# Performance work log

Measured on AMD Instinct MI355X. Metric: run time of the kernel, lower is better.

## Reference

```python
import jax, jax.numpy as jnp
import numpy as np

B, T, I, H, O = 1024, 512, 4, 128, 4


def setup_inputs() -> dict:
    key = jax.random.key(0)
    ks = jax.random.split(key, 7)
    s_ih = 1.0 / np.sqrt(H)
    return {
        "x": jax.random.normal(ks[0], (B, T, I), dtype=jnp.float32),
        "W_ih": jax.random.uniform(ks[1], (4 * H, I), jnp.float32, -s_ih, s_ih),
        "W_hh": jax.random.uniform(ks[2], (4 * H, H), jnp.float32, -s_ih, s_ih),
        "b_ih": jax.random.uniform(ks[3], (4 * H,), jnp.float32, -s_ih, s_ih),
        "b_hh": jax.random.uniform(ks[4], (4 * H,), jnp.float32, -s_ih, s_ih),
        "W_fc": jax.random.uniform(ks[5], (O, H), jnp.float32, -s_ih, s_ih),
        "b_fc": jax.random.uniform(ks[6], (O,), jnp.float32, -s_ih, s_ih),
    }


def _lstm_last_hidden(x, W_ih, W_hh, b_ih, b_hh):
    """Single-layer LSTM (PyTorch gate order i,f,g,o); returns h_T of shape (B,H)."""
    Bn = x.shape[0]
    Hn = W_hh.shape[1]
    # Precompute input contributions for all timesteps: (T, B, 4H)
    x_proj = jnp.einsum('bti,gi->tbg', x, W_ih) + (b_ih + b_hh)

    def step(carry, xp_t):
        h, c = carry
        gates = xp_t + h @ W_hh.T  # (B, 4H)
        i_g, f_g, g_g, o_g = jnp.split(gates, 4, axis=-1)
        i_g = jax.nn.sigmoid(i_g)
        f_g = jax.nn.sigmoid(f_g)
        g_g = jnp.tanh(g_g)
        o_g = jax.nn.sigmoid(o_g)
        c = f_g * c + i_g * g_g
        h = o_g * jnp.tanh(c)
        return (h, c), None

    h0 = jnp.zeros((Bn, Hn), x.dtype)
    c0 = jnp.zeros((Bn, Hn), x.dtype)
    (h_T, _), _ = jax.lax.scan(step, (h0, c0), x_proj)
    return h_T


def reference(x, W_ih, W_hh, b_ih, b_hh, W_fc, b_fc):
    # out, _ = lstm(x); last = out[:, -1]; dropout (eval/identity); fc(last)
    last = _lstm_last_hidden(x, W_ih, W_hh, b_ih, b_hh)
    return last @ W_fc.T + b_fc
```

## Files before the change

kernel.cpp:

```cpp
#include <hip/hip_runtime.h>
#include <hip/hip_bf16.h>


#define Tlen 512
#define Iin  4
#define Hdim 128
#define Odim 4

#define SB0() __builtin_amdgcn_sched_barrier(0)

typedef __attribute__((ext_vector_type(8))) short bf16x8;
typedef __attribute__((ext_vector_type(4))) float f32x4;
typedef __attribute__((ext_vector_type(2))) unsigned uint2v;
typedef __attribute__((ext_vector_type(4))) unsigned uint4v;

static __device__ __forceinline__ short f2bf(float f) {
  union { float f; unsigned u; } v; v.f = f;
  unsigned u = v.u;
  return (short)((u + 0x7FFFu + ((u >> 16) & 1u)) >> 16);
}
static __device__ __forceinline__ unsigned cvt_pk_bf16(float lo, float hi) {
  unsigned r;
  asm("v_cvt_pk_bf16_f32 %0, %1, %2" : "=v"(r) : "v"(lo), "v"(hi));
  return r;
}
static __device__ __forceinline__ float ex2(float x) { return __builtin_amdgcn_exp2f(x); }
static __device__ __forceinline__ float rcp_(float x) { return __builtin_amdgcn_rcpf(x); }

#define MFMA __builtin_amdgcn_mfma_f32_16x16x32_bf16

__global__ __launch_bounds__(512) void lstm_kernel(
    const float* __restrict__ x, const float* __restrict__ W_ih,
    const float* __restrict__ W_hh, const float* __restrict__ b_ih,
    const float* __restrict__ b_hh, const float* __restrict__ W_fc,
    const float* __restrict__ b_fc, float* __restrict__ out) {
  __shared__ alignas(16) short Albuf[2][16][168];
  __shared__ float hfin[16][Hdim];

  const int tid  = threadIdx.x;
  const int wid  = tid >> 6;
  const int lane = tid & 63;
  const int m16  = lane & 15;
  const int grp  = lane >> 4;
  const int bbase = blockIdx.x * 16;
  const float L2E = 1.4426950408889634f;

  bf16x8 Wf[4][4];
  bf16x8 Wx[4];
  f32x4  c0v[4];
#pragma unroll
  for (int q = 0; q < 4; ++q) {
    const float sc = (q == 2) ? 2.0f * L2E : L2E;
    const int gm = q * 128 + wid * 16 + m16;
#pragma unroll
    for (int kc = 0; kc < 4; ++kc) {
      const float* src = W_hh + (size_t)gm * Hdim + kc * 32 + grp * 8;
      bf16x8 w;
#pragma unroll
      for (int e = 0; e < 8; ++e) w[e] = f2bf(src[e] * sc);
      Wf[q][kc] = w;
    }
    bf16x8 w4 = {0, 0, 0, 0, 0, 0, 0, 0};
    if (grp == 0) {
#pragma unroll
      for (int e = 0; e < 4; ++e) w4[e] = f2bf(W_ih[gm * Iin + e] * sc);
    }
    Wx[q] = w4;
#pragma unroll
    for (int r = 0; r < 4; ++r) {
      const int gr = q * 128 + wid * 16 + grp * 4 + r;
      c0v[q][r] = (b_ih[gr] + b_hh[gr]) * sc;
    }
  }

  for (int i = tid; i < 2 * 16 * 168; i += 512) ((short*)Albuf)[i] = 0;

  const float* xrow = x + (size_t)(bbase + m16) * (Tlen * Iin);

  f32x4 acc0, acc1, acc2, acc3;
  {
    f32x4 xv = *(const f32x4*)xrow;
    uint4v u;
    u[0] = cvt_pk_bf16(xv[0], xv[1]);
    u[1] = cvt_pk_bf16(xv[2], xv[3]);
    u[2] = 0; u[3] = 0;
    union { uint4v uu; bf16x8 v; } cst; cst.uu = u;
    acc0 = MFMA(Wx[0], cst.v, c0v[0], 0, 0, 0);
    acc1 = MFMA(Wx[1], cst.v, c0v[1], 0, 0, 0);
    acc2 = MFMA(Wx[2], cst.v, c0v[2], 0, 0, 0);
    acc3 = MFMA(Wx[3], cst.v, c0v[3], 0, 0, 0);
  }

  float c4[4] = {0.f, 0.f, 0.f, 0.f};
  float hl[4] = {0.f, 0.f, 0.f, 0.f};
  __syncthreads();

  for (int t = 0; t < Tlen; ++t) {
    const int cur = t & 1, nxt = cur ^ 1;

    bf16x8 b0 = *(const bf16x8*)&Albuf[cur][m16][ 0 + grp * 8];
    bf16x8 b1 = *(const bf16x8*)&Albuf[cur][m16][32 + grp * 8];
    bf16x8 b2 = *(const bf16x8*)&Albuf[cur][m16][64 + grp * 8];
    bf16x8 b3 = *(const bf16x8*)&Albuf[cur][m16][96 + grp * 8];
    const int tn = (t + 1 < Tlen) ? (t + 1) : (Tlen - 1);
    f32x4 xv = *(const f32x4*)(xrow + (size_t)tn * Iin);

    acc0 = MFMA(Wf[0][0], b0, acc0, 0, 0, 0);
    acc0 = MFMA(Wf[0][1], b1, acc0, 0, 0, 0);
    acc0 = MFMA(Wf[0][2], b2, acc0, 0, 0, 0);
    acc0 = MFMA(Wf[0][3], b3, acc0, 0, 0, 0);
    acc1 = MFMA(Wf[1][0], b0, acc1, 0, 0, 0);
    acc1 = MFMA(Wf[1][1], b1, acc1, 0, 0, 0);
    acc1 = MFMA(Wf[1][2], b2, acc1, 0, 0, 0);
    acc1 = MFMA(Wf[1][3], b3, acc1, 0, 0, 0);
    SB0();
    f32x4 si;
    {
      float p0 = 1.0f + ex2(-acc0[0]), p1 = 1.0f + ex2(-acc0[1]);
      float p2 = 1.0f + ex2(-acc0[2]), p3 = 1.0f + ex2(-acc0[3]);
      float r01 = rcp_(p0 * p1), r23 = rcp_(p2 * p3);
      si[0] = r01 * p1; si[1] = r01 * p0; si[2] = r23 * p3; si[3] = r23 * p2;
    }
    SB0();
    acc2 = MFMA(Wf[2][0], b0, acc2, 0, 0, 0);
    acc2 = MFMA(Wf[2][1], b1, acc2, 0, 0, 0);
    acc2 = MFMA(Wf[2][2], b2, acc2, 0, 0, 0);
    acc2 = MFMA(Wf[2][3], b3, acc2, 0, 0, 0);
    SB0();
    f32x4 sf;
    {
      float p0 = 1.0f + ex2(-acc1[0]), p1 = 1.0f + ex2(-acc1[1]);
      float p2 = 1.0f + ex2(-acc1[2]), p3 = 1.0f + ex2(-acc1[3]);
      float r01 = rcp_(p0 * p1), r23 = rcp_(p2 * p3);
      sf[0] = r01 * p1; sf[1] = r01 * p0; sf[2] = r23 * p3; sf[3] = r23 * p2;
    }
    SB0();
    acc3 = MFMA(Wf[3][0], b0, acc3, 0, 0, 0);
    acc3 = MFMA(Wf[3][1], b1, acc3, 0, 0, 0);
    acc3 = MFMA(Wf[3][2], b2, acc3, 0, 0, 0);
    acc3 = MFMA(Wf[3][3], b3, acc3, 0, 0, 0);
    SB0();
    f32x4 gt;
    {
      float p0 = 1.0f + ex2(-acc2[0]), p1 = 1.0f + ex2(-acc2[1]);
      float p2 = 1.0f + ex2(-acc2[2]), p3 = 1.0f + ex2(-acc2[3]);
      float r01 = rcp_(p0 * p1), r23 = rcp_(p2 * p3);
      float r01_2 = r01 + r01, r23_2 = r23 + r23;
      gt[0] = __builtin_fmaf(r01_2, p1, -1.0f);
      gt[1] = __builtin_fmaf(r01_2, p0, -1.0f);
      gt[2] = __builtin_fmaf(r23_2, p3, -1.0f);
      gt[3] = __builtin_fmaf(r23_2, p2, -1.0f);
    }
    SB0();
    f32x4 so;
    {
      float p0 = 1.0f + ex2(-acc3[0]), p1 = 1.0f + ex2(-acc3[1]);
      float p2 = 1.0f + ex2(-acc3[2]), p3 = 1.0f + ex2(-acc3[3]);
      float r01 = rcp_(p0 * p1), r23 = rcp_(p2 * p3);
      so[0] = r01 * p1; so[1] = r01 * p0; so[2] = r23 * p3; so[3] = r23 * p2;
    }

#pragma unroll
    for (int r = 0; r < 4; ++r)
      c4[r] = __builtin_fmaf(sf[r], c4[r], si[r] * gt[r]);
    {
      float p0 = 1.0f + ex2(-2.8853900817779268f * c4[0]);
      float p1 = 1.0f + ex2(-2.8853900817779268f * c4[1]);
      float p2 = 1.0f + ex2(-2.8853900817779268f * c4[2]);
      float p3 = 1.0f + ex2(-2.8853900817779268f * c4[3]);
      float r01 = rcp_(p0 * p1), r23 = rcp_(p2 * p3);
      float r01_2 = r01 + r01, r23_2 = r23 + r23;
      hl[0] = so[0] * __builtin_fmaf(r01_2, p1, -1.0f);
      hl[1] = so[1] * __builtin_fmaf(r01_2, p0, -1.0f);
      hl[2] = so[2] * __builtin_fmaf(r23_2, p3, -1.0f);
      hl[3] = so[3] * __builtin_fmaf(r23_2, p2, -1.0f);
    }

    uint2v hp;
    hp[0] = cvt_pk_bf16(hl[0], hl[1]);
    hp[1] = cvt_pk_bf16(hl[2], hl[3]);
    *(uint2v*)&Albuf[nxt][m16][wid * 16 + grp * 4] = hp;

    {
      uint4v u;
      u[0] = cvt_pk_bf16(xv[0], xv[1]);
      u[1] = cvt_pk_bf16(xv[2], xv[3]);
      u[2] = 0; u[3] = 0;
      union { uint4v uu; bf16x8 v; } cst; cst.uu = u;
      acc0 = MFMA(Wx[0], cst.v, c0v[0], 0, 0, 0);
      acc1 = MFMA(Wx[1], cst.v, c0v[1], 0, 0, 0);
      acc2 = MFMA(Wx[2], cst.v, c0v[2], 0, 0, 0);
      acc3 = MFMA(Wx[3], cst.v, c0v[3], 0, 0, 0);
    }

    __syncthreads();
  }

  {
    f32x4 hv;
    hv[0] = hl[0]; hv[1] = hl[1]; hv[2] = hl[2]; hv[3] = hl[3];
    *(f32x4*)&hfin[m16][wid * 16 + grp * 4] = hv;
  }
  __syncthreads();
  if (tid < 64) {
    const int row = tid >> 2, o = tid & 3;
    float s = b_fc[o];
#pragma unroll 8
    for (int k = 0; k < Hdim; ++k) s += hfin[row][k] * W_fc[o * Hdim + k];
    out[(size_t)(bbase + row) * Odim + o] = s;
  }
}

extern "C" void kernel_launch(void* const* d_in, const int* in_sizes, int n_in,
                              void* d_out, int out_size, void* d_ws, size_t ws_size,
                              hipStream_t stream) {
  const float* x    = (const float*)d_in[0];
  const float* W_ih = (const float*)d_in[1];
  const float* W_hh = (const float*)d_in[2];
  const float* b_ih = (const float*)d_in[3];
  const float* b_hh = (const float*)d_in[4];
  const float* W_fc = (const float*)d_in[5];
  const float* b_fc = (const float*)d_in[6];
  float* out = (float*)d_out;
  lstm_kernel<<<64, 512, 0, stream>>>(x, W_ih, W_hh, b_ih, b_hh, W_fc, b_fc, out);
}
```

Measured before the change: 371.5 us.

## Interleave two independent batch tiles per block to overlap MFMA with gate math

Each block now processes 32 batch rows as two independent 16-row tiles, A and B, staggered by half a timestep. The MFMA recurrence of one tile is interleaved with the sigmoid/tanh gate math of the other, so matrix and vector work can overlap instead of serialising on the dependency chain. The grid is halved to 32 blocks, and there are now two barriers per timestep. This trades half the parallelism across CUs for better latency hiding inside each block.

```diff
diff --git a/kernel.cpp b/kernel.cpp
--- a/kernel.cpp
+++ b/kernel.cpp
@@ -34,15 +34,16 @@
     const float* __restrict__ W_hh, const float* __restrict__ b_ih,
     const float* __restrict__ b_hh, const float* __restrict__ W_fc,
     const float* __restrict__ b_fc, float* __restrict__ out) {
-  __shared__ alignas(16) short Albuf[2][16][168];
-  __shared__ float hfin[16][Hdim];
+  __shared__ alignas(16) short bufA[16][168];
+  __shared__ alignas(16) short bufB[16][168];
+  __shared__ float hfin[32][Hdim];
 
   const int tid  = threadIdx.x;
   const int wid  = tid >> 6;
   const int lane = tid & 63;
   const int m16  = lane & 15;
   const int grp  = lane >> 4;
-  const int bbase = blockIdx.x * 16;
+  const int bbase = blockIdx.x * 32;
   const float L2E = 1.4426950408889634f;
 
   bf16x8 Wf[4][4];
@@ -73,77 +74,269 @@
     }
   }
 
-  for (int i = tid; i < 2 * 16 * 168; i += 512) ((short*)Albuf)[i] = 0;
-
-  const float* xrow = x + (size_t)(bbase + m16) * (Tlen * Iin);
-
-  f32x4 acc0, acc1, acc2, acc3;
+  for (int i = tid; i < 16 * 168; i += 512) {
+    ((short*)bufA)[i] = 0;
+    ((short*)bufB)[i] = 0;
+  }
+
+  const float* xrowA = x + (size_t)(bbase + m16) * (Tlen * Iin);
+  const float* xrowB = xrowA + (size_t)16 * (Tlen * Iin);
+
+  f32x4 accA0, accA1, accA2, accA3, accB0, accB1, accB2, accB3;
   {
-    f32x4 xv = *(const f32x4*)xrow;
+    f32x4 xa = *(const f32x4*)xrowA;
     uint4v u;
-    u[0] = cvt_pk_bf16(xv[0], xv[1]);
-    u[1] = cvt_pk_bf16(xv[2], xv[3]);
+    u[0] = cvt_pk_bf16(xa[0], xa[1]);
+    u[1] = cvt_pk_bf16(xa[2], xa[3]);
     u[2] = 0; u[3] = 0;
     union { uint4v uu; bf16x8 v; } cst; cst.uu = u;
-    acc0 = MFMA(Wx[0], cst.v, c0v[0], 0, 0, 0);
-    acc1 = MFMA(Wx[1], cst.v, c0v[1], 0, 0, 0);
-    acc2 = MFMA(Wx[2], cst.v, c0v[2], 0, 0, 0);
-    acc3 = MFMA(Wx[3], cst.v, c0v[3], 0, 0, 0);
-  }
-
-  float c4[4] = {0.f, 0.f, 0.f, 0.f};
-  float hl[4] = {0.f, 0.f, 0.f, 0.f};
+    accA0 = MFMA(Wx[0], cst.v, c0v[0], 0, 0, 0);
+    accA1 = MFMA(Wx[1], cst.v, c0v[1], 0, 0, 0);
+    accA2 = MFMA(Wx[2], cst.v, c0v[2], 0, 0, 0);
+    accA3 = MFMA(Wx[3], cst.v, c0v[3], 0, 0, 0);
+  }
+  {
+    f32x4 xb = *(const f32x4*)xrowB;
+    uint4v u;
+    u[0] = cvt_pk_bf16(xb[0], xb[1]);
+    u[1] = cvt_pk_bf16(xb[2], xb[3]);
+    u[2] = 0; u[3] = 0;
+    union { uint4v uu; bf16x8 v; } cst; cst.uu = u;
+    accB0 = MFMA(Wx[0], cst.v, c0v[0], 0, 0, 0);
+    accB1 = MFMA(Wx[1], cst.v, c0v[1], 0, 0, 0);
+    accB2 = MFMA(Wx[2], cst.v, c0v[2], 0, 0, 0);
+    accB3 = MFMA(Wx[3], cst.v, c0v[3], 0, 0, 0);
+  }
+
+  float c4A[4] = {0.f, 0.f, 0.f, 0.f};
+  float c4B[4] = {0.f, 0.f, 0.f, 0.f};
+  float hlA[4] = {0.f, 0.f, 0.f, 0.f};
+  float hlB[4] = {0.f, 0.f, 0.f, 0.f};
   __syncthreads();
 
+  {
+    bf16x8 a0 = *(const bf16x8*)&bufA[m16][ 0 + grp * 8];
+    bf16x8 a1 = *(const bf16x8*)&bufA[m16][32 + grp * 8];
+    bf16x8 a2 = *(const bf16x8*)&bufA[m16][64 + grp * 8];
+    bf16x8 a3 = *(const bf16x8*)&bufA[m16][96 + grp * 8];
+    accA0 = MFMA(Wf[0][0], a0, accA0, 0, 0, 0);
+    accA1 = MFMA(Wf[1][0], a0, accA1, 0, 0, 0);
+    accA2 = MFMA(Wf[2][0], a0, accA2, 0, 0, 0);
+    accA3 = MFMA(Wf[3][0], a0, accA3, 0, 0, 0);
+    accA0 = MFMA(Wf[0][1], a1, accA0, 0, 0, 0);
+    accA1 = MFMA(Wf[1][1], a1, accA1, 0, 0, 0);
+    accA2 = MFMA(Wf[2][1], a1, accA2, 0, 0, 0);
+    accA3 = MFMA(Wf[3][1], a1, accA3, 0, 0, 0);
+    accA0 = MFMA(Wf[0][2], a2, accA0, 0, 0, 0);
+    accA1 = MFMA(Wf[1][2], a2, accA1, 0, 0, 0);
+    accA2 = MFMA(Wf[2][2], a2, accA2, 0, 0, 0);
+    accA3 = MFMA(Wf[3][2], a2, accA3, 0, 0, 0);
+    accA0 = MFMA(Wf[0][3], a3, accA0, 0, 0, 0);
+    accA1 = MFMA(Wf[1][3], a3, accA1, 0, 0, 0);
+    accA2 = MFMA(Wf[2][3], a3, accA2, 0, 0, 0);
+    accA3 = MFMA(Wf[3][3], a3, accA3, 0, 0, 0);
+  }
+  __syncthreads();
+
   for (int t = 0; t < Tlen; ++t) {
-    const int cur = t & 1, nxt = cur ^ 1;
-
-    bf16x8 b0 = *(const bf16x8*)&Albuf[cur][m16][ 0 + grp * 8];
-    bf16x8 b1 = *(const bf16x8*)&Albuf[cur][m16][32 + grp * 8];
-    bf16x8 b2 = *(const bf16x8*)&Albuf[cur][m16][64 + grp * 8];
-    bf16x8 b3 = *(const bf16x8*)&Albuf[cur][m16][96 + grp * 8];
-    const int tn = (t + 1 < Tlen) ? (t + 1) : (Tlen - 1);
-    f32x4 xv = *(const f32x4*)(xrow + (size_t)tn * Iin);
-
-    acc0 = MFMA(Wf[0][0], b0, acc0, 0, 0, 0);
-    acc0 = MFMA(Wf[0][1], b1, acc0, 0, 0, 0);
-    acc0 = MFMA(Wf[0][2], b2, acc0, 0, 0, 0);
-    acc0 = MFMA(Wf[0][3], b3, acc0, 0, 0, 0);
-    acc1 = MFMA(Wf[1][0], b0, acc1, 0, 0, 0);
-    acc1 = MFMA(Wf[1][1], b1, acc1, 0, 0, 0);
-    acc1 = MFMA(Wf[1][2], b2, acc1, 0, 0, 0);
-    acc1 = MFMA(Wf[1][3], b3, acc1, 0, 0, 0);
-    SB0();
-    f32x4 si;
-    {
-      float p0 = 1.0f + ex2(-acc0[0]), p1 = 1.0f + ex2(-acc0[1]);
-      float p2 = 1.0f + ex2(-acc0[2]), p3 = 1.0f + ex2(-acc0[3]);
+    {
+      bf16x8 v0 = *(const bf16x8*)&bufB[m16][ 0 + grp * 8];
+      bf16x8 v1 = *(const bf16x8*)&bufB[m16][32 + grp * 8];
+      bf16x8 v2 = *(const bf16x8*)&bufB[m16][64 + grp * 8];
+      bf16x8 v3 = *(const bf16x8*)&bufB[m16][96 + grp * 8];
+      const int tnA = (t + 1 < Tlen) ? (t + 1) : (Tlen - 1);
+      f32x4 xvA = *(const f32x4*)(xrowA + (size_t)tnA * Iin);
+
+      accB0 = MFMA(Wf[0][0], v0, accB0, 0, 0, 0);
+      accB1 = MFMA(Wf[1][0], v0, accB1, 0, 0, 0);
+      accB2 = MFMA(Wf[2][0], v0, accB2, 0, 0, 0);
+      accB3 = MFMA(Wf[3][0], v0, accB3, 0, 0, 0);
+      SB0();
+      float Ai0 = 1.0f + ex2(-accA0[0]), Ai1 = 1.0f + ex2(-accA0[1]);
+      float Ai2 = 1.0f + ex2(-accA0[2]), Ai3 = 1.0f + ex2(-accA0[3]);
+      float Af0 = 1.0f + ex2(-accA1[0]), Af1 = 1.0f + ex2(-accA1[1]);
+      float Af2 = 1.0f + ex2(-accA1[2]), Af3 = 1.0f + ex2(-accA1[3]);
+      SB0();
+      accB0 = MFMA(Wf[0][1], v1, accB0, 0, 0, 0);
+      accB1 = MFMA(Wf[1][1], v1, accB1, 0, 0, 0);
+      accB2 = MFMA(Wf[2][1], v1, accB2, 0, 0, 0);
+      accB3 = MFMA(Wf[3][1], v1, accB3, 0, 0, 0);
+      SB0();
+      f32x4 si, sf;
+      {
+        float r01 = rcp_(Ai0 * Ai1), r23 = rcp_(Ai2 * Ai3);
+        si[0] = r01 * Ai1; si[1] = r01 * Ai0; si[2] = r23 * Ai3; si[3] = r23 * Ai2;
+        float q01 = rcp_(Af0 * Af1), q23 = rcp_(Af2 * Af3);
+        sf[0] = q01 * Af1; sf[1] = q01 * Af0; sf[2] = q23 * Af3; sf[3] = q23 * Af2;
+      }
+      SB0();
+      accB0 = MFMA(Wf[0][2], v2, accB0, 0, 0, 0);
+      accB1 = MFMA(Wf[1][2], v2, accB1, 0, 0, 0);
+      accB2 = MFMA(Wf[2][2], v2, accB2, 0, 0, 0);
+      accB3 = MFMA(Wf[3][2], v2, accB3, 0, 0, 0);
+      SB0();
+      f32x4 gt, so;
+      {
+        float p0 = 1.0f + ex2(-accA2[0]), p1 = 1.0f + ex2(-accA2[1]);
+        float p2 = 1.0f + ex2(-accA2[2]), p3 = 1.0f + ex2(-accA2[3]);
+        float r01 = rcp_(p0 * p1), r23 = rcp_(p2 * p3);
+        float r01_2 = r01 + r01, r23_2 = r23 + r23;
+        gt[0] = __builtin_fmaf(r01_2, p1, -1.0f);
+        gt[1] = __builtin_fmaf(r01_2, p0, -1.0f);
+        gt[2] = __builtin_fmaf(r23_2, p3, -1.0f);
+        gt[3] = __builtin_fmaf(r23_2, p2, -1.0f);
+        float s0 = 1.0f + ex2(-accA3[0]), s1 = 1.0f + ex2(-accA3[1]);
+        float s2 = 1.0f + ex2(-accA3[2]), s3 = 1.0f + ex2(-accA3[3]);
+        float u01 = rcp_(s0 * s1), u23 = rcp_(s2 * s3);
+        so[0] = u01 * s1; so[1] = u01 * s0; so[2] = u23 * s3; so[3] = u23 * s2;
+      }
+      SB0();
+      accB0 = MFMA(Wf[0][3], v3, accB0, 0, 0, 0);
+      accB1 = MFMA(Wf[1][3], v3, accB1, 0, 0, 0);
+      accB2 = MFMA(Wf[2][3], v3, accB2, 0, 0, 0);
+      accB3 = MFMA(Wf[3][3], v3, accB3, 0, 0, 0);
+      SB0();
+#pragma unroll
+      for (int r = 0; r < 4; ++r)
+        c4A[r] = __builtin_fmaf(sf[r], c4A[r], si[r] * gt[r]);
+      {
+        float p0 = 1.0f + ex2(-2.8853900817779268f * c4A[0]);
+        float p1 = 1.0f + ex2(-2.8853900817779268f * c4A[1]);
+        float p2 = 1.0f + ex2(-2.8853900817779268f * c4A[2]);
+        float p3 = 1.0f + ex2(-2.8853900817779268f * c4A[3]);
+        float r01 = rcp_(p0 * p1), r23 = rcp_(p2 * p3);
+        float r01_2 = r01 + r01, r23_2 = r23 + r23;
+        hlA[0] = so[0] * __builtin_fmaf(r01_2, p1, -1.0f);
+        hlA[1] = so[1] * __builtin_fmaf(r01_2, p0, -1.0f);
+        hlA[2] = so[2] * __builtin_fmaf(r23_2, p3, -1.0f);
+        hlA[3] = so[3] * __builtin_fmaf(r23_2, p2, -1.0f);
+      }
+      uint2v hp;
+      hp[0] = cvt_pk_bf16(hlA[0], hlA[1]);
+      hp[1] = cvt_pk_bf16(hlA[2], hlA[3]);
+      *(uint2v*)&bufA[m16][wid * 16 + grp * 4] = hp;
+      {
+        uint4v u;
+        u[0] = cvt_pk_bf16(xvA[0], xvA[1]);
+        u[1] = cvt_pk_bf16(xvA[2], xvA[3]);
+        u[2] = 0; u[3] = 0;
+        union { uint4v uu; bf16x8 v; } cst; cst.uu = u;
+        accA0 = MFMA(Wx[0], cst.v, c0v[0], 0, 0, 0);
+        accA1 = MFMA(Wx[1], cst.v, c0v[1], 0, 0, 0);
+        accA2 = MFMA(Wx[2], cst.v, c0v[2], 0, 0, 0);
+        accA3 = MFMA(Wx[3], cst.v, c0v[3], 0, 0, 0);
+      }
+    }
+    __syncthreads();
+
+    if (t + 1 < Tlen) {
+      const int tt = t + 1;
+      bf16x8 a0 = *(const bf16x8*)&bufA[m16][ 0 + grp * 8];
+      bf16x8 a1 = *(const bf16x8*)&bufA[m16][32 + grp * 8];
+      bf16x8 a2 = *(const bf16x8*)&bufA[m16][64 + grp * 8];
+      bf16x8 a3 = *(const bf16x8*)&bufA[m16][96 + grp * 8];
+      f32x4 xvB = *(const f32x4*)(xrowB + (size_t)tt * Iin);
+
+      accA0 = MFMA(Wf[0][0], a0, accA0, 0, 0, 0);
+      accA1 = MFMA(Wf[1][0], a0, accA1, 0, 0, 0);
+      accA2 = MFMA(Wf[2][0], a0, accA2, 0, 0, 0);
+      accA3 = MFMA(Wf[3][0], a0, accA3, 0, 0, 0);
+      SB0();
+      float Bi0 = 1.0f + ex2(-accB0[0]), Bi1 = 1.0f + ex2(-accB0[1]);
+      float Bi2 = 1.0f + ex2(-accB0[2]), Bi3 = 1.0f + ex2(-accB0[3]);
+      float Bf0 = 1.0f + ex2(-accB1[0]), Bf1 = 1.0f + ex2(-accB1[1]);
+      float Bf2 = 1.0f + ex2(-accB1[2]), Bf3 = 1.0f + ex2(-accB1[3]);
+      SB0();
+      accA0 = MFMA(Wf[0][1], a1, accA0, 0, 0, 0);
+      accA1 = MFMA(Wf[1][1], a1, accA1, 0, 0, 0);
+      accA2 = MFMA(Wf[2][1], a1, accA2, 0, 0, 0);
+      accA3 = MFMA(Wf[3][1], a1, accA3, 0, 0, 0);
+      SB0();
+      f32x4 si, sf;
+      {
+        float r01 = rcp_(Bi0 * Bi1), r23 = rcp_(Bi2 * Bi3);
+        si[0] = r01 * Bi1; si[1] = r01 * Bi0; si[2] = r23 * Bi3; si[3] = r23 * Bi2;
+        float q01 = rcp_(Bf0 * Bf1), q23 = rcp_(Bf2 * Bf3);
+        sf[0] = q01 * Bf1; sf[1] = q01 * Bf0; sf[2] = q23 * Bf3; sf[3] = q23 * Bf2;
+      }
+      SB0();
+      accA0 = MFMA(Wf[0][2], a2, accA0, 0, 0, 0);
+      accA1 = MFMA(Wf[1][2], a2, accA1, 0, 0, 0);
+      accA2 = MFMA(Wf[2][2], a2, accA2, 0, 0, 0);
+      accA3 = MFMA(Wf[3][2], a2, accA3, 0, 0, 0);
+      SB0();
+      f32x4 gt, so;
+      {
+        float p0 = 1.0f + ex2(-accB2[0]), p1 = 1.0f + ex2(-accB2[1]);
+        float p2 = 1.0f + ex2(-accB2[2]), p3 = 1.0f + ex2(-accB2[3]);
+        float r01 = rcp_(p0 * p1), r23 = rcp_(p2 * p3);
+        float r01_2 = r01 + r01, r23_2 = r23 + r23;
+        gt[0] = __builtin_fmaf(r01_2, p1, -1.0f);
+        gt[1] = __builtin_fmaf(r01_2, p0, -1.0f);
+        gt[2] = __builtin_fmaf(r23_2, p3, -1.0f);
+        gt[3] = __builtin_fmaf(r23_2, p2, -1.0f);
+        float s0 = 1.0f + ex2(-accB3[0]), s1 = 1.0f + ex2(-accB3[1]);
+        float s2 = 1.0f + ex2(-accB3[2]), s3 = 1.0f + ex2(-accB3[3]);
+        float u01 = rcp_(s0 * s1), u23 = rcp_(s2 * s3);
+        so[0] = u01 * s1; so[1] = u01 * s0; so[2] = u23 * s3; so[3] = u23 * s2;
+      }
+      SB0();
+      accA0 = MFMA(Wf[0][3], a3, accA0, 0, 0, 0);
+      accA1 = MFMA(Wf[1][3], a3, accA1, 0, 0, 0);
+      accA2 = MFMA(Wf[2][3], a3, accA2, 0, 0, 0);
+      accA3 = MFMA(Wf[3][3], a3, accA3, 0, 0, 0);
+      SB0();
+#pragma unroll
+      for (int r = 0; r < 4; ++r)
+        c4B[r] = __builtin_fmaf(sf[r], c4B[r], si[r] * gt[r]);
+      {
+        float p0 = 1.0f + ex2(-2.8853900817779268f * c4B[0]);
+        float p1 = 1.0f + ex2(-2.8853900817779268f * c4B[1]);
+        float p2 = 1.0f + ex2(-2.8853900817779268f * c4B[2]);
+        float p3 = 1.0f + ex2(-2.8853900817779268f * c4B[3]);
+        float r01 = rcp_(p0 * p1), r23 = rcp_(p2 * p3);
+        float r01_2 = r01 + r01, r23_2 = r23 + r23;
+        hlB[0] = so[0] * __builtin_fmaf(r01_2, p1, -1.0f);
+        hlB[1] = so[1] * __builtin_fmaf(r01_2, p0, -1.0f);
+        hlB[2] = so[2] * __builtin_fmaf(r23_2, p3, -1.0f);
+        hlB[3] = so[3] * __builtin_fmaf(r23_2, p2, -1.0f);
+      }
+      uint2v hp;
+      hp[0] = cvt_pk_bf16(hlB[0], hlB[1]);
+      hp[1] = cvt_pk_bf16(hlB[2], hlB[3]);
+      *(uint2v*)&bufB[m16][wid * 16 + grp * 4] = hp;
+      {
+        uint4v u;
+        u[0] = cvt_pk_bf16(xvB[0], xvB[1]);
+        u[1] = cvt_pk_bf16(xvB[2], xvB[3]);
+        u[2] = 0; u[3] = 0;
+        union { uint4v uu; bf16x8 v; } cst; cst.uu = u;
+        accB0 = MFMA(Wx[0], cst.v, c0v[0], 0, 0, 0);
+        accB1 = MFMA(Wx[1], cst.v, c0v[1], 0, 0, 0);
+        accB2 = MFMA(Wx[2], cst.v, c0v[2], 0, 0, 0);
+        accB3 = MFMA(Wx[3], cst.v, c0v[3], 0, 0, 0);
+      }
+      __syncthreads();
+    }
+  }
+
+  {
+    f32x4 si, sf, gt, so;
+    {
+      float p0 = 1.0f + ex2(-accB0[0]), p1 = 1.0f + ex2(-accB0[1]);
+      float p2 = 1.0f + ex2(-accB0[2]), p3 = 1.0f + ex2(-accB0[3]);
       float r01 = rcp_(p0 * p1), r23 = rcp_(p2 * p3);
       si[0] = r01 * p1; si[1] = r01 * p0; si[2] = r23 * p3; si[3] = r23 * p2;
     }
-    SB0();
-    acc2 = MFMA(Wf[2][0], b0, acc2, 0, 0, 0);
-    acc2 = MFMA(Wf[2][1], b1, acc2, 0, 0, 0);
-    acc2 = MFMA(Wf[2][2], b2, acc2, 0, 0, 0);
-    acc2 = MFMA(Wf[2][3], b3, acc2, 0, 0, 0);
-    SB0();
-    f32x4 sf;
-    {
-      float p0 = 1.0f + ex2(-acc1[0]), p1 = 1.0f + ex2(-acc1[1]);
-      float p2 = 1.0f + ex2(-acc1[2]), p3 = 1.0f + ex2(-acc1[3]);
+    {
+      float p0 = 1.0f + ex2(-accB1[0]), p1 = 1.0f + ex2(-accB1[1]);
+      float p2 = 1.0f + ex2(-accB1[2]), p3 = 1.0f + ex2(-accB1[3]);
       float r01 = rcp_(p0 * p1), r23 = rcp_(p2 * p3);
       sf[0] = r01 * p1; sf[1] = r01 * p0; sf[2] = r23 * p3; sf[3] = r23 * p2;
     }
-    SB0();
-    acc3 = MFMA(Wf[3][0], b0, acc3, 0, 0, 0);
-    acc3 = MFMA(Wf[3][1], b1, acc3, 0, 0, 0);
-    acc3 = MFMA(Wf[3][2], b2, acc3, 0, 0, 0);
-    acc3 = MFMA(Wf[3][3], b3, acc3, 0, 0, 0);
-    SB0();
-    f32x4 gt;
-    {
-      float p0 = 1.0f + ex2(-acc2[0]), p1 = 1.0f + ex2(-acc2[1]);
-      float p2 = 1.0f + ex2(-acc2[2]), p3 = 1.0f + ex2(-acc2[3]);
+    {
+      float p0 = 1.0f + ex2(-accB2[0]), p1 = 1.0f + ex2(-accB2[1]);
+      float p2 = 1.0f + ex2(-accB2[2]), p3 = 1.0f + ex2(-accB2[3]);
       float r01 = rcp_(p0 * p1), r23 = rcp_(p2 * p3);
       float r01_2 = r01 + r01, r23_2 = r23 + r23;
       gt[0] = __builtin_fmaf(r01_2, p1, -1.0f);
@@ -151,58 +344,39 @@
       gt[2] = __builtin_fmaf(r23_2, p3, -1.0f);
       gt[3] = __builtin_fmaf(r23_2, p2, -1.0f);
     }
-    SB0();
-    f32x4 so;
-    {
-      float p0 = 1.0f + ex2(-acc3[0]), p1 = 1.0f + ex2(-acc3[1]);
-      float p2 = 1.0f + ex2(-acc3[2]), p3 = 1.0f + ex2(-acc3[3]);
+    {
+      float p0 = 1.0f + ex2(-accB3[0]), p1 = 1.0f + ex2(-accB3[1]);
+      float p2 = 1.0f + ex2(-accB3[2]), p3 = 1.0f + ex2(-accB3[3]);
       float r01 = rcp_(p0 * p1), r23 = rcp_(p2 * p3);
       so[0] = r01 * p1; so[1] = r01 * p0; so[2] = r23 * p3; so[3] = r23 * p2;
     }
-
 #pragma unroll
     for (int r = 0; r < 4; ++r)
-      c4[r] = __builtin_fmaf(sf[r], c4[r], si[r] * gt[r]);
-    {
-      float p0 = 1.0f + ex2(-2.8853900817779268f * c4[0]);
-      float p1 = 1.0f + ex2(-2.8853900817779268f * c4[1]);
-      float p2 = 1.0f + ex2(-2.8853900817779268f * c4[2]);
-      float p3 = 1.0f + ex2(-2.8853900817779268f * c4[3]);
+      c4B[r] = __builtin_fmaf(sf[r], c4B[r], si[r] * gt[r]);
+    {
+      float p0 = 1.0f + ex2(-2.8853900817779268f * c4B[0]);
+      float p1 = 1.0f + ex2(-2.8853900817779268f * c4B[1]);
+      float p2 = 1.0f + ex2(-2.8853900817779268f * c4B[2]);
+      float p3 = 1.0f + ex2(-2.8853900817779268f * c4B[3]);
       float r01 = rcp_(p0 * p1), r23 = rcp_(p2 * p3);
       float r01_2 = r01 + r01, r23_2 = r23 + r23;
-      hl[0] = so[0] * __builtin_fmaf(r01_2, p1, -1.0f);
-      hl[1] = so[1] * __builtin_fmaf(r01_2, p0, -1.0f);
-      hl[2] = so[2] * __builtin_fmaf(r23_2, p3, -1.0f);
-      hl[3] = so[3] * __builtin_fmaf(r23_2, p2, -1.0f);
-    }
-
-    uint2v hp;
-    hp[0] = cvt_pk_bf16(hl[0], hl[1]);
-    hp[1] = cvt_pk_bf16(hl[2], hl[3]);
-    *(uint2v*)&Albuf[nxt][m16][wid * 16 + grp * 4] = hp;
-
-    {
-      uint4v u;
-      u[0] = cvt_pk_bf16(xv[0], xv[1]);
-      u[1] = cvt_pk_bf16(xv[2], xv[3]);
-      u[2] = 0; u[3] = 0;
-      union { uint4v uu; bf16x8 v; } cst; cst.uu = u;
-      acc0 = MFMA(Wx[0], cst.v, c0v[0], 0, 0, 0);
-      acc1 = MFMA(Wx[1], cst.v, c0v[1], 0, 0, 0);
-      acc2 = MFMA(Wx[2], cst.v, c0v[2], 0, 0, 0);
-      acc3 = MFMA(Wx[3], cst.v, c0v[3], 0, 0, 0);
-    }
-
-    __syncthreads();
+      hlB[0] = so[0] * __builtin_fmaf(r01_2, p1, -1.0f);
+      hlB[1] = so[1] * __builtin_fmaf(r01_2, p0, -1.0f);
+      hlB[2] = so[2] * __builtin_fmaf(r23_2, p3, -1.0f);
+      hlB[3] = so[3] * __builtin_fmaf(r23_2, p2, -1.0f);
+    }
   }
 
   {
     f32x4 hv;
-    hv[0] = hl[0]; hv[1] = hl[1]; hv[2] = hl[2]; hv[3] = hl[3];
+    hv[0] = hlA[0]; hv[1] = hlA[1]; hv[2] = hlA[2]; hv[3] = hlA[3];
     *(f32x4*)&hfin[m16][wid * 16 + grp * 4] = hv;
+    f32x4 hw;
+    hw[0] = hlB[0]; hw[1] = hlB[1]; hw[2] = hlB[2]; hw[3] = hlB[3];
+    *(f32x4*)&hfin[16 + m16][wid * 16 + grp * 4] = hw;
   }
   __syncthreads();
-  if (tid < 64) {
+  if (tid < 128) {
     const int row = tid >> 2, o = tid & 3;
     float s = b_fc[o];
 #pragma unroll 8
@@ -222,5 +396,5 @@
   const float* W_fc = (const float*)d_in[5];
   const float* b_fc = (const float*)d_in[6];
   float* out = (float*)d_out;
-  lstm_kernel<<<64, 512, 0, stream>>>(x, W_ih, W_hh, b_ih, b_hh, W_fc, b_fc, out);
+  lstm_kernel<<<32, 512, 0, stream>>>(x, W_ih, W_hh, b_ih, b_hh, W_fc, b_fc, out);
 }
```

After: 703.2 us. 89.3% more time.
